# Kernel tuning notes

Hardware: AMD Instinct MI355X
Metric: run time of the kernel (lower is better)

## Reference

```python
import jax, jax.numpy as jnp
import numpy as np

N = 4096      # nodes (= maxlen)
E = 4096      # hyperedges
NFEAT = 512
NHID = 512
NHEAD = 8
DK = 64
DV = 64
NLAYER = 4
NCLASS = 16
GAMMA = 0.5
LN_EPS = 1e-5


def _incidence(key):
    # sparse-ish binary incidence matrix with no empty rows/cols
    H = (jax.random.uniform(key, (N, E)) < 0.004).astype(jnp.float32)
    H = H.at[jnp.arange(N), jnp.arange(N) % E].set(1.0)   # every node in >=1 edge
    H = H.at[jnp.arange(E) % N, jnp.arange(E)].set(1.0)   # every edge has >=1 node
    return H


def setup_inputs() -> dict:
    key = jax.random.key(0)
    ks = jax.random.split(key, 16)
    s = 0.02
    inp = {
        "X0": jax.random.normal(ks[0], (N, NFEAT), jnp.float32),
        "H": _incidence(ks[1]),
        "w_feat": jax.random.normal(ks[2], (NFEAT, NHID), jnp.float32) * s,
        "b_feat": jnp.zeros((NHID,), jnp.float32),
        "Wq": jax.random.normal(ks[3], (NLAYER, NHID, NHEAD * DK), jnp.float32) * s,
        "bq": jnp.zeros((NLAYER, NHEAD * DK), jnp.float32),
        "Wk": jax.random.normal(ks[4], (NLAYER, NHID, NHEAD * DK), jnp.float32) * s,
        "bk": jnp.zeros((NLAYER, NHEAD * DK), jnp.float32),
        "Wv": jax.random.normal(ks[5], (NLAYER, NHID, NHEAD * DV), jnp.float32) * s,
        "bv": jnp.zeros((NLAYER, NHEAD * DV), jnp.float32),
        "Wo": jax.random.normal(ks[6], (NLAYER, NHEAD * DV, NHID), jnp.float32) * s,
        "bo": jnp.zeros((NLAYER, NHID), jnp.float32),
        "ln_g": jnp.ones((NLAYER, NHID), jnp.float32),
        "ln_b": jnp.zeros((NLAYER, NHID), jnp.float32),
        "prelu_a": jnp.full((NLAYER,), 0.25, jnp.float32),
        "w_cls": jax.random.normal(ks[7], (NHID, NCLASS), jnp.float32) * s,
        "b_cls": jnp.zeros((NCLASS,), jnp.float32),
    }
    return inp


def _laplace(H):
    # G = DV^-1/2 H W DE^-1 H^T DV^-1/2 with W = I (diag matmuls as broadcasts)
    DV_ = jnp.sum(H, axis=1)                 # [N]
    DE_ = jnp.sum(H, axis=0)                 # [E]
    dv2 = DV_ ** -0.5
    dv2 = dv2.at[0].set(1.0)                 # DV2[0,0] = 1 quirk
    M = (H * (1.0 / DE_)[None, :]) @ H.T     # [N, N]
    return dv2[:, None] * M * dv2[None, :]


def _layer_norm(x, g, b):
    mu = jnp.mean(x, axis=-1, keepdims=True)
    var = jnp.mean((x - mu) ** 2, axis=-1, keepdims=True)
    return (x - mu) * jax.lax.rsqrt(var + LN_EPS) * g + b


def _encoder_layer(x, G, Wq, bq, Wk, bk, Wv, bv, Wo, bo, g, b, a):
    n = x.shape[0]
    q = (x @ Wq + bq).reshape(n, NHEAD, DK)
    k = (x @ Wk + bk).reshape(n, NHEAD, DK)
    v = (x @ Wv + bv).reshape(n, NHEAD, DV)
    scores = jnp.einsum("nhd,mhd->hnm", q, k) / np.sqrt(DK).astype(np.float32)
    attn = jax.nn.softmax(scores, axis=-1)                       # [h, n, n]
    blend = attn * GAMMA + G[None, :, :] * (1.0 - GAMMA)
    ctx = jnp.einsum("hnm,mhd->nhd", blend, v).reshape(n, NHEAD * DV)
    out = _layer_norm(ctx @ Wo + bo + x, g, b)                   # residual = V = x
    out = jnp.where(out >= 0, out, a * out)                      # PReLU (scalar a)
    return out  # dropout is identity at eval


def reference(X0, H, w_feat, b_feat, Wq, bq, Wk, bk, Wv, bv, Wo, bo,
              ln_g, ln_b, prelu_a, w_cls, b_cls):
    G = _laplace(H)
    x = X0 @ w_feat + b_feat
    for i in range(NLAYER):
        x = _encoder_layer(x, G, Wq[i], bq[i], Wk[i], bk[i], Wv[i], bv[i],
                           Wo[i], bo[i], ln_g[i], ln_b[i], prelu_a[i])
    logits = x @ w_cls + b_cls
    return jax.nn.log_softmax(logits, axis=1)
```

## Files before the change

### kernel.cpp

```cpp
#include <hip/hip_runtime.h>
#include <stdint.h>
#include <stddef.h>

typedef unsigned short u16;
typedef __attribute__((ext_vector_type(8))) short short8;
typedef __attribute__((ext_vector_type(4))) float floatx4;

#define NN 4096
#define FD 512
#define NLAYER 4
#define NCLASS 16

__device__ __forceinline__ float b2f(u16 u) {
  union { unsigned int i; float f; } x; x.i = ((unsigned int)u) << 16; return x.f;
}
__device__ __forceinline__ u16 f2b(float f) {
  union { float f; unsigned int i; } x; x.f = f;
  unsigned int r = x.i + 0x7fffu + ((x.i >> 16) & 1u);
  return (u16)(r >> 16);
}
__device__ __forceinline__ int is_f32(const void* Hraw) {
  return ((const u16*)Hraw)[0] == 0;
}
__device__ __forceinline__ float rload(const void* p, size_t i, int f) {
  if (f) { union { unsigned int i; float x; } u; u.i = ((const unsigned int*)p)[i]; return u.x; }
  return b2f(((const u16*)p)[i]);
}
__device__ __forceinline__ void gl2lds16(const void* g, void* l) {
  __builtin_amdgcn_global_load_lds((const __attribute__((address_space(1))) void*)g,
                                   (__attribute__((address_space(3))) void*)l, 16, 0, 0);
}

__global__ __launch_bounds__(256) void gemm_qkv(
    const u16* __restrict__ A, const u16* __restrict__ B, u16* __restrict__ qk,
    u16* __restrict__ vb, u16* __restrict__ vT, int K, long boff,
    const void* __restrict__ bq, const void* __restrict__ bk, const void* __restrict__ bv,
    const void* __restrict__ Hflag)
{
  __shared__ __align__(16) u16 As[64 * 32];
  __shared__ __align__(16) u16 Bs[128 * 32];
  __shared__ u16 Ts[4][16 * 17];
  const int tid = threadIdx.x;
  const int wave = tid >> 6, lane = tid & 63;
  const int wr = (wave >> 1) * 32, wc = (wave & 1) * 64;
  const int srow = lane >> 2;
  const int scol = (((lane & 3) ^ (srow & 3)) * 8);
  const int q4 = lane >> 4, l15 = lane & 15;
  const int sg = l15 & 3;

  floatx4 acc[2][4] = {};
  const u16* Ag = A + (size_t)(blockIdx.y * 64) * K;
  const u16* Bg = B + (size_t)(blockIdx.x * 128) * K;

  for (int k0 = 0; k0 < K; k0 += 32) {
    gl2lds16(Ag + (size_t)(wave * 16 + srow) * K + k0 + scol, &As[wave * 512]);
#pragma unroll
    for (int t = 0; t < 2; t++) {
      const int s = wave * 2 + t;
      gl2lds16(Bg + (size_t)(s * 16 + srow) * K + k0 + scol, &Bs[s * 512]);
    }
    __syncthreads();
    short8 af[2], bf[4];
#pragma unroll
    for (int mt = 0; mt < 2; mt++)
      af[mt] = *(const short8*)&As[(wr + mt * 16 + l15) * 32 + ((q4 ^ sg) * 8)];
#pragma unroll
    for (int nt = 0; nt < 4; nt++)
      bf[nt] = *(const short8*)&Bs[(wc + nt * 16 + l15) * 32 + ((q4 ^ sg) * 8)];
#pragma unroll
    for (int mt = 0; mt < 2; mt++)
#pragma unroll
      for (int nt = 0; nt < 4; nt++)
        acc[mt][nt] = __builtin_amdgcn_mfma_f32_16x16x32_bf16(af[mt], bf[nt], acc[mt][nt], 0, 0, 0);
    __syncthreads();
  }

  const int fl = is_f32(Hflag);
  const int buf = blockIdx.x >> 2;
  const void* bptr = (buf == 0) ? bq : (buf == 1) ? bk : bv;
  const int colbase = (blockIdx.x & 3) * 128;
  const int rowblk = blockIdx.y * 64;

  if (buf < 2) {
    u16* out = qk + (size_t)buf * 2097152;
#pragma unroll
    for (int mt = 0; mt < 2; mt++)
#pragma unroll
      for (int nt = 0; nt < 4; nt++)
#pragma unroll
        for (int r = 0; r < 4; r++) {
          const int row = rowblk + wr + mt * 16 + q4 * 4 + r;
          const int col = colbase + wc + nt * 16 + l15;
          out[(size_t)row * 512 + col] = f2b(acc[mt][nt][r] + rload(bptr, (size_t)boff + col, fl));
        }
  } else {
#pragma unroll
    for (int mt = 0; mt < 2; mt++)
#pragma unroll
      for (int nt = 0; nt < 4; nt++) {
#pragma unroll
        for (int r = 0; r < 4; r++) {
          const int row = rowblk + wr + mt * 16 + q4 * 4 + r;
          const int col = colbase + wc + nt * 16 + l15;
          const u16 val = f2b(acc[mt][nt][r] + rload(bptr, (size_t)boff + col, fl));
          vb[(size_t)row * 512 + col] = val;
          Ts[wave][(q4 * 4 + r) * 17 + l15] = val;
        }
#pragma unroll
        for (int r = 0; r < 4; r++) {
          const u16 tv = Ts[wave][l15 * 17 + q4 * 4 + r];
          const int vrow = colbase + wc + nt * 16 + q4 * 4 + r;
          const int vcol = rowblk + wr + mt * 16 + l15;
          vT[(size_t)vrow * NN + vcol] = tv;
        }
      }
  }
}

template<int EP>
__global__ __launch_bounds__(256) void gemm64_bt(
    const u16* __restrict__ A, const u16* __restrict__ B, u16* __restrict__ C,
    int M, int N, int K,
    const void* __restrict__ bias, long boff,
    const u16* __restrict__ add,
    const void* __restrict__ Hflag)
{
  __shared__ __align__(16) u16 As[64 * 32];
  __shared__ __align__(16) u16 Bs[128 * 32];
  const int tid = threadIdx.x;
  const int wave = tid >> 6, lane = tid & 63;
  const int wr = (wave >> 1) * 32, wc = (wave & 1) * 64;
  const int srow = lane >> 2;
  const int scol = (((lane & 3) ^ (srow & 3)) * 8);
  const int q4 = lane >> 4, l15 = lane & 15;
  const int sg = l15 & 3;

  floatx4 acc[2][4] = {};
  const u16* Ag = A + (size_t)(blockIdx.y * 64) * K;
  const u16* Bg = B + (size_t)(blockIdx.x * 128) * K;

  for (int k0 = 0; k0 < K; k0 += 32) {
    gl2lds16(Ag + (size_t)(wave * 16 + srow) * K + k0 + scol, &As[wave * 512]);
#pragma unroll
    for (int t = 0; t < 2; t++) {
      const int s = wave * 2 + t;
      gl2lds16(Bg + (size_t)(s * 16 + srow) * K + k0 + scol, &Bs[s * 512]);
    }
    __syncthreads();
    short8 af[2], bf[4];
#pragma unroll
    for (int mt = 0; mt < 2; mt++)
      af[mt] = *(const short8*)&As[(wr + mt * 16 + l15) * 32 + ((q4 ^ sg) * 8)];
#pragma unroll
    for (int nt = 0; nt < 4; nt++)
      bf[nt] = *(const short8*)&Bs[(wc + nt * 16 + l15) * 32 + ((q4 ^ sg) * 8)];
#pragma unroll
    for (int mt = 0; mt < 2; mt++)
#pragma unroll
      for (int nt = 0; nt < 4; nt++)
        acc[mt][nt] = __builtin_amdgcn_mfma_f32_16x16x32_bf16(af[mt], bf[nt], acc[mt][nt], 0, 0, 0);
    __syncthreads();
  }

  const int fl = is_f32(Hflag);
#pragma unroll
  for (int mt = 0; mt < 2; mt++)
#pragma unroll
    for (int nt = 0; nt < 4; nt++)
#pragma unroll
      for (int r = 0; r < 4; r++) {
        const int row = blockIdx.y * 64 + wr + mt * 16 + q4 * 4 + r;
        const int col = blockIdx.x * 128 + wc + nt * 16 + l15;
        float v = acc[mt][nt][r];
        if (EP == 2) v += rload(bias, (size_t)boff + col, fl);
        if (EP == 4) v += rload(bias, (size_t)boff + col, fl) + b2f(add[(size_t)row * N + col]);
        C[(size_t)row * N + col] = f2b(v);
      }
}

__global__ __launch_bounds__(256) void flash_attn(
    const u16* __restrict__ q, const u16* __restrict__ k,
    const u16* __restrict__ vT, u16* __restrict__ O0, u16* __restrict__ O1,
    float* __restrict__ lp)
{
  __shared__ __align__(16) u16 Qs[128 * 64];
  __shared__ __align__(16) u16 Ks[2][64 * 64], Vs[2][64 * 64];
  __shared__ __align__(16) u16 Ps[4][32 * 72];
  const int tid = threadIdx.x, wave = tid >> 6, lane = tid & 63;
  const int h = blockIdx.y, q0 = blockIdx.x * 128, z = blockIdx.z;
  const int jbase = z * 2048;
  const int r8 = lane >> 3;
  const int c8 = (((lane & 7) ^ r8) * 8);
  const int q4 = lane >> 4, l15 = lane & 15;
  const int sw = l15 & 7;

#pragma unroll
  for (int t = 0; t < 4; t++) {
    const int s = wave * 4 + t;
    gl2lds16(q + (size_t)(q0 + s * 8 + r8) * FD + h * 64 + c8, &Qs[s * 512]);
  }
#pragma unroll
  for (int t = 0; t < 2; t++) {
    const int s = wave * 2 + t;
    gl2lds16(k + (size_t)(jbase + s * 8 + r8) * FD + h * 64 + c8, &Ks[0][s * 512]);
    gl2lds16(vT + (size_t)(h * 64 + s * 8 + r8) * NN + jbase + c8, &Vs[0][s * 512]);
  }
  __syncthreads();
  short8 aq[2][2];
#pragma unroll
  for (int mt = 0; mt < 2; mt++) {
    aq[mt][0] = *(const short8*)&Qs[(wave * 32 + mt * 16 + l15) * 64 + ((q4 ^ sw) * 8)];
    aq[mt][1] = *(const short8*)&Qs[(wave * 32 + mt * 16 + l15) * 64 + (((q4 + 4) ^ sw) * 8)];
  }
  short8 vone;
#pragma unroll
  for (int j = 0; j < 8; j++) vone[j] = (short)0x3F80;

  floatx4 O[2][4] = {};
  floatx4 lacc[2] = {};

  for (int jt = 0; jt < 32; jt++) {
    const int cur = jt & 1;
    if (jt + 1 < 32) {
      const int nb = cur ^ 1;
      const int j0 = jbase + (jt + 1) * 64;
#pragma unroll
      for (int t = 0; t < 2; t++) {
        const int s = wave * 2 + t;
        gl2lds16(k + (size_t)(j0 + s * 8 + r8) * FD + h * 64 + c8, &Ks[nb][s * 512]);
        gl2lds16(vT + (size_t)(h * 64 + s * 8 + r8) * NN + j0 + c8, &Vs[nb][s * 512]);
      }
    }
    floatx4 sacc[2][4] = {};
#pragma unroll
    for (int nt = 0; nt < 4; nt++) {
      const short8 bk0 = *(const short8*)&Ks[cur][(nt * 16 + l15) * 64 + ((q4 ^ sw) * 8)];
      const short8 bk1 = *(const short8*)&Ks[cur][(nt * 16 + l15) * 64 + (((q4 + 4) ^ sw) * 8)];
#pragma unroll
      for (int mt = 0; mt < 2; mt++) {
        sacc[mt][nt] = __builtin_amdgcn_mfma_f32_16x16x32_bf16(aq[mt][0], bk0, sacc[mt][nt], 0, 0, 0);
        sacc[mt][nt] = __builtin_amdgcn_mfma_f32_16x16x32_bf16(aq[mt][1], bk1, sacc[mt][nt], 0, 0, 0);
      }
    }
#pragma unroll
    for (int mt = 0; mt < 2; mt++)
#pragma unroll
      for (int nt = 0; nt < 4; nt++)
#pragma unroll
        for (int r = 0; r < 4; r++) {
          const float pv = __expf(fmaf(sacc[mt][nt][r], 0.125f, -10.f));
          Ps[wave][(mt * 16 + q4 * 4 + r) * 72 + nt * 16 + l15] =
              (u16)(__float_as_uint(pv) >> 16);
        }
#pragma unroll
    for (int kk = 0; kk < 2; kk++) {
      short8 ap[2];
#pragma unroll
      for (int mt = 0; mt < 2; mt++)
        ap[mt] = *(const short8*)&Ps[wave][(mt * 16 + l15) * 72 + kk * 32 + q4 * 8];
#pragma unroll
      for (int dt = 0; dt < 4; dt++) {
        const short8 bv = *(const short8*)&Vs[cur][(dt * 16 + l15) * 64 + (((kk * 4 + q4) ^ sw) * 8)];
#pragma unroll
        for (int mt = 0; mt < 2; mt++)
          O[mt][dt] = __builtin_amdgcn_mfma_f32_16x16x32_bf16(ap[mt], bv, O[mt][dt], 0, 0, 0);
      }
#pragma unroll
      for (int mt = 0; mt < 2; mt++)
        lacc[mt] = __builtin_amdgcn_mfma_f32_16x16x32_bf16(ap[mt], vone, lacc[mt], 0, 0, 0);
    }
    __syncthreads();
  }
  u16* Op = z ? O1 : O0;
#pragma unroll
  for (int mt = 0; mt < 2; mt++) {
#pragma unroll
    for (int dt = 0; dt < 4; dt++)
#pragma unroll
      for (int r = 0; r < 4; r++)
        Op[(size_t)(q0 + wave * 32 + mt * 16 + q4 * 4 + r) * FD + h * 64 + dt * 16 + l15] =
            f2b(O[mt][dt][r]);
    if (l15 == 0)
#pragma unroll
      for (int r = 0; r < 4; r++)
        lp[z * 32768 + h * 4096 + q0 + wave * 32 + mt * 16 + q4 * 4 + r] = lacc[mt][r];
  }
}

__global__ __launch_bounds__(256) void spmm_edge(
    const int* __restrict__ offC, const int* __restrict__ nodeList,
    const float* __restrict__ invDE, const float* __restrict__ dv2,
    const u16* __restrict__ vb, float* __restrict__ b)
{
  const int wave = threadIdx.x >> 6, lane = threadIdx.x & 63;
  const int e = blockIdx.x * 4 + wave;
  const int beg = offC[e], end = offC[e + 1];
  float acc[8] = {};
  for (int j = beg; j < end; j++) {
    const int i = nodeList[j];
    const float dvi = dv2[i];
    const short8 row = *(const short8*)&vb[(size_t)i * 512 + lane * 8];
#pragma unroll
    for (int t = 0; t < 8; t++) acc[t] += dvi * b2f((u16)row[t]);
  }
  const float s = invDE[e];
  float4* out = (float4*)&b[(size_t)e * 512 + lane * 8];
  float4 o0, o1;
  o0.x = acc[0] * s; o0.y = acc[1] * s; o0.z = acc[2] * s; o0.w = acc[3] * s;
  o1.x = acc[4] * s; o1.y = acc[5] * s; o1.z = acc[6] * s; o1.w = acc[7] * s;
  out[0] = o0; out[1] = o1;
}

__global__ __launch_bounds__(256) void spmm_node(
    const int* __restrict__ offR, const int* __restrict__ edgeList,
    const float* __restrict__ dv2, const float* __restrict__ b,
    const u16* __restrict__ O0, const u16* __restrict__ O1,
    const float* __restrict__ lp, u16* __restrict__ ctx)
{
  const int wave = threadIdx.x >> 6, lane = threadIdx.x & 63;
  const int i = blockIdx.x * 4 + wave;
  const int beg = offR[i], end = offR[i + 1];
  float acc[8] = {};
  for (int j = beg; j < end; j++) {
    const int e = edgeList[j];
    const float4* bp = (const float4*)&b[(size_t)e * 512 + lane * 8];
    const float4 b0 = bp[0], b1 = bp[1];
    acc[0] += b0.x; acc[1] += b0.y; acc[2] += b0.z; acc[3] += b0.w;
    acc[4] += b1.x; acc[5] += b1.y; acc[6] += b1.z; acc[7] += b1.w;
  }
  const int h = lane >> 3;
  const float invl = 1.f / (lp[h * 4096 + i] + lp[32768 + h * 4096 + i]);
  const float dvi = dv2[i];
  const short8 a0 = *(const short8*)&O0[(size_t)i * 512 + lane * 8];
  const short8 a1 = *(const short8*)&O1[(size_t)i * 512 + lane * 8];
  short8 o;
#pragma unroll
  for (int t = 0; t < 8; t++)
    o[t] = (short)f2b(0.5f * (dvi * acc[t] + (b2f((u16)a0[t]) + b2f((u16)a1[t])) * invl));
  *(short8*)&ctx[(size_t)i * 512 + lane * 8] = o;
}

__global__ __launch_bounds__(256) void degrees_pass1(
    const void* __restrict__ H, float* __restrict__ colpart,
    float* __restrict__ rowsum) {
  __shared__ float cs[NN];
  __shared__ float wsum[16][4];
  const int f = is_f32(H);
  const int tid = threadIdx.x, wave = tid >> 6, lane = tid & 63;
  for (int i = tid; i < NN; i += 256) cs[i] = 0.f;
  __syncthreads();
  const int r0 = blockIdx.x * 16;
  for (int rr = 0; rr < 16; rr++) {
    const size_t rowbase = (size_t)(r0 + rr) * NN;
    float rs = 0.f;
#pragma unroll
    for (int j = 0; j < 16; j++) {
      const int c = tid + j * 256;
      const float v = rload(H, rowbase + c, f);
      cs[c] += v;
      rs += v;
    }
#pragma unroll
    for (int off = 1; off < 64; off <<= 1) rs += __shfl_xor(rs, off);
    if (lane == 0) wsum[rr][wave] = rs;
  }
  __syncthreads();
  if (tid < 16)
    rowsum[r0 + tid] = wsum[tid][0] + wsum[tid][1] + wsum[tid][2] + wsum[tid][3];
  float* cp = colpart + (size_t)blockIdx.x * NN;
  for (int i = tid; i < NN; i += 256) cp[i] = cs[i];
}

__global__ __launch_bounds__(256) void finalize_degrees(
    const float* __restrict__ colpart, float* __restrict__ invDE,
    const float* __restrict__ rowsum, float* __restrict__ dv2,
    float* __restrict__ colsum) {
  __shared__ float red[4][64];
  const int tid = threadIdx.x;
  const int c = tid & 63, pc = tid >> 6;
  const int col = blockIdx.x * 64 + c;
  float s = 0.f;
  for (int p = pc * 64; p < pc * 64 + 64; p++) s += colpart[(size_t)p * NN + col];
  red[pc][c] = s;
  const int r = blockIdx.x * 256 + tid;
  if (r < NN) dv2[r] = (r == 0) ? 1.f : rsqrtf(rowsum[r]);
  __syncthreads();
  if (pc == 0) {
    const float tot = red[0][c] + red[1][c] + red[2][c] + red[3][c];
    colsum[col] = tot;
    invDE[col] = 1.f / tot;
  }
}

__global__ __launch_bounds__(256) void build_offsets(
    const float* __restrict__ rowsum, const float* __restrict__ colsum,
    int* __restrict__ offR, int* __restrict__ offC,
    int* __restrict__ curR, int* __restrict__ curC)
{
  __shared__ int part[256];
  const int tid = threadIdx.x;
  for (int half = 0; half < 2; half++) {
    const float* src = half ? colsum : rowsum;
    int* off = half ? offC : offR;
    int* cur = half ? curC : curR;
    int local[16]; int s = 0;
#pragma unroll
    for (int j = 0; j < 16; j++) { local[j] = s; s += (int)(src[tid * 16 + j] + 0.5f); }
    part[tid] = s;
    __syncthreads();
    for (int d = 1; d < 256; d <<= 1) {
      const int v = (tid >= d) ? part[tid - d] : 0;
      __syncthreads();
      part[tid] += v;
      __syncthreads();
    }
    const int pre = (tid == 0) ? 0 : part[tid - 1];
#pragma unroll
    for (int j = 0; j < 16; j++) {
      const int o = pre + local[j];
      off[tid * 16 + j] = o;
      cur[tid * 16 + j] = o;
    }
    if (tid == 255) off[4096] = part[255];
    __syncthreads();
  }
}

__global__ void fill_csr(const void* __restrict__ H,
                         int* __restrict__ curR, int* __restrict__ curC,
                         int* __restrict__ edgeList, int* __restrict__ nodeList)
{
  const int f = is_f32(H);
  const size_t g = (size_t)blockIdx.x * 256 + threadIdx.x;
  const size_t stride = (size_t)gridDim.x * 256;
  for (size_t idx = g; idx < (size_t)NN * NN; idx += stride) {
    if (rload(H, idx, f) != 0.f) {
      const int i = (int)(idx >> 12);
      const int e = (int)(idx & (NN - 1));
      edgeList[atomicAdd(&curR[i], 1)] = e;
      nodeList[atomicAdd(&curC[e], 1)] = i;
    }
  }
}

__global__ __launch_bounds__(256) void transpose_cvt(
    const void* __restrict__ in, long eoff, u16* __restrict__ out, int R, int C,
    const void* __restrict__ Hflag) {
  __shared__ u16 tile[32][33];
  const int f = is_f32(Hflag);
  const int tx = threadIdx.x & 31, ty = threadIdx.x >> 5;
  const int bx = blockIdx.x, by = blockIdx.y;
#pragma unroll
  for (int kk = 0; kk < 4; kk++)
    tile[ty + kk * 8][tx] =
        f2b(rload(in, (size_t)eoff + (size_t)(by * 32 + ty + kk * 8) * C + bx * 32 + tx, f));
  __syncthreads();
#pragma unroll
  for (int kk = 0; kk < 4; kk++)
    out[(size_t)(bx * 32 + ty + kk * 8) * R + by * 32 + tx] = tile[tx][ty + kk * 8];
}

__global__ __launch_bounds__(256) void transpose_cvt4(
    const void* __restrict__ Wq, const void* __restrict__ Wk,
    const void* __restrict__ Wv, const void* __restrict__ Wo,
    long eoff, u16* __restrict__ wTs, const void* __restrict__ Hflag) {
  __shared__ u16 tile[32][33];
  const int z = blockIdx.z;
  const void* in = (z == 0) ? Wq : (z == 1) ? Wk : (z == 2) ? Wv : Wo;
  u16* out = wTs + (size_t)z * 262144;
  const int f = is_f32(Hflag);
  const int tx = threadIdx.x & 31, ty = threadIdx.x >> 5;
  const int bx = blockIdx.x, by = blockIdx.y;
#pragma unroll
  for (int kk = 0; kk < 4; kk++)
    tile[ty + kk * 8][tx] =
        f2b(rload(in, (size_t)eoff + (size_t)(by * 32 + ty + kk * 8) * 512 + bx * 32 + tx, f));
  __syncthreads();
#pragma unroll
  for (int kk = 0; kk < 4; kk++)
    out[(size_t)(bx * 32 + ty + kk * 8) * 512 + by * 32 + tx] = tile[tx][ty + kk * 8];
}

__global__ void convert_flat(const void* __restrict__ in, u16* __restrict__ out, int n,
                             const void* __restrict__ Hflag) {
  const int f = is_f32(Hflag);
  const int g = blockIdx.x * 256 + threadIdx.x;
  const int stride = gridDim.x * 256;
  for (int i = g; i < n; i += stride) out[i] = f2b(rload(in, i, f));
}

__global__ __launch_bounds__(256) void ln_prelu(
    const u16* __restrict__ pre, const void* __restrict__ g, const void* __restrict__ bb,
    const void* __restrict__ aa, int lidx, u16* __restrict__ X,
    const void* __restrict__ Hflag) {
  const int f = is_f32(Hflag);
  const int tid = threadIdx.x, wave = tid >> 6, lane = tid & 63;
  const int row = blockIdx.x * 4 + wave;
  const short8 raw = *(const short8*)(pre + (size_t)row * FD + lane * 8);
  float v[8], s = 0.f;
#pragma unroll
  for (int j = 0; j < 8; j++) { v[j] = b2f((u16)raw[j]); s += v[j]; }
#pragma unroll
  for (int off = 1; off < 64; off <<= 1) s += __shfl_xor(s, off);
  const float mu = s * (1.f / 512.f);
  float vs = 0.f;
#pragma unroll
  for (int j = 0; j < 8; j++) { const float d = v[j] - mu; vs += d * d; }
#pragma unroll
  for (int off = 1; off < 64; off <<= 1) vs += __shfl_xor(vs, off);
  const float rstd = rsqrtf(vs * (1.f / 512.f) + 1e-5f);
  const float a = rload(aa, lidx, f);
  short8 o;
#pragma unroll
  for (int j = 0; j < 8; j++) {
    float y = (v[j] - mu) * rstd * rload(g, (size_t)lidx * 512 + lane * 8 + j, f)
              + rload(bb, (size_t)lidx * 512 + lane * 8 + j, f);
    y = (y >= 0.f) ? y : a * y;
    o[j] = (short)f2b(y);
  }
  *(short8*)(X + (size_t)row * FD + lane * 8) = o;
}

__global__ __launch_bounds__(256) void cls_logsoftmax(
    const u16* __restrict__ X, const void* __restrict__ w, const void* __restrict__ bc,
    void* __restrict__ out, const void* __restrict__ Hflag) {
  __shared__ float wsm[FD * NCLASS];
  const int f = is_f32(Hflag);
  const int tid = threadIdx.x;
  for (int i = tid; i < FD * NCLASS; i += 256) wsm[i] = rload(w, i, f);
  __syncthreads();
  const int c = tid & 15;
  const int row = blockIdx.x * 16 + (tid >> 4);
  const u16* x = X + (size_t)row * FD;
  float z = rload(bc, c, f);
  for (int kk = 0; kk < FD; kk++) z += b2f(x[kk]) * wsm[kk * NCLASS + c];
  float mx = z;
#pragma unroll
  for (int off = 1; off < 16; off <<= 1) mx = fmaxf(mx, __shfl_xor(mx, off));
  float se = __expf(z - mx);
#pragma unroll
  for (int off = 1; off < 16; off <<= 1) se += __shfl_xor(se, off);
  const float val = z - mx - logf(se);
  if (f) ((float*)out)[(size_t)row * NCLASS + c] = val;
  else   ((u16*)out)[(size_t)row * NCLASS + c] = f2b(val);
}

extern "C" void kernel_launch(void* const* d_in, const int* in_sizes, int n_in,
                              void* d_out, int out_size, void* d_ws, size_t ws_size,
                              hipStream_t stream) {
  const void* X0     = d_in[0];
  const void* H      = d_in[1];
  const void* w_feat = d_in[2];
  const void* b_feat = d_in[3];
  const void* Wq     = d_in[4];
  const void* bq     = d_in[5];
  const void* Wk     = d_in[6];
  const void* bk     = d_in[7];
  const void* Wv     = d_in[8];
  const void* bv     = d_in[9];
  const void* Wo     = d_in[10];
  const void* bo     = d_in[11];
  const void* ln_g   = d_in[12];
  const void* ln_b   = d_in[13];
  const void* pa     = d_in[14];
  const void* w_cls  = d_in[15];
  const void* b_cls  = d_in[16];

  char* ws = (char*)d_ws;
  char* r1 = ws;
  int* offR      = (int*)(r1 + (0 << 10));
  int* offC      = (int*)(r1 + (32 << 10));
  int* curR      = (int*)(r1 + (64 << 10));
  int* curC      = (int*)(r1 + (96 << 10));
  int* edgeList  = (int*)(r1 + ((size_t)1 << 20));
  int* nodeList  = (int*)(r1 + ((size_t)4 << 20));
  float* bbuf    = (float*)(r1 + ((size_t)8 << 20));
  u16* vb        = (u16*)(r1 + ((size_t)16 << 20));
  float* colpart = (float*)(r1 + ((size_t)20 << 20));

  char* r2  = ws + ((size_t)32 << 20);
  u16* qb     = (u16*)(r2 + ((size_t)0  << 20));
  u16* Opart0 = (u16*)(r2 + ((size_t)8  << 20));
  u16* vTb    = (u16*)(r2 + ((size_t)12 << 20));
  u16* ctx    = (u16*)(r2 + ((size_t)16 << 20));
  u16* X      = (u16*)(r2 + ((size_t)20 << 20));
  u16* wTs    = (u16*)(r2 + ((size_t)24 << 20));
  u16* Opart1 = (u16*)(r2 + ((size_t)26 << 20));
  float* lpart = (float*)(r2 + ((size_t)30 << 20));
  u16* opre = qb;
  u16* X0b  = Opart0;

  float* dv2    = (float*)d_out;
  float* invDE  = dv2 + 4096;
  float* rowsum = dv2 + 8192;
  float* colsum = dv2 + 12288;

  degrees_pass1<<<256, 256, 0, stream>>>(H, colpart, rowsum);
  finalize_degrees<<<64, 256, 0, stream>>>(colpart, invDE, rowsum, dv2, colsum);
  build_offsets<<<1, 256, 0, stream>>>(rowsum, colsum, offR, offC, curR, curC);
  fill_csr<<<2048, 256, 0, stream>>>(H, curR, curC, edgeList, nodeList);

  convert_flat<<<2048, 256, 0, stream>>>(X0, X0b, NN * FD, H);
  transpose_cvt<<<dim3(16, 16), 256, 0, stream>>>(w_feat, 0, wTs, 512, 512, H);
  gemm64_bt<2><<<dim3(4, 64), 256, 0, stream>>>(X0b, wTs, X, NN, FD, FD, b_feat, 0, nullptr, H);

  for (int l = 0; l < NLAYER; l++) {
    const long lw = (long)l * 262144;
    transpose_cvt4<<<dim3(16, 16, 4), 256, 0, stream>>>(Wq, Wk, Wv, Wo, lw, wTs, H);

    gemm_qkv<<<dim3(12, 64), 256, 0, stream>>>(X, wTs, qb, vb, vTb, FD, (long)l * 512, bq, bk, bv, H);
    flash_attn<<<dim3(32, 8, 2), 256, 0, stream>>>(qb, qb + 2097152, vTb, Opart0, Opart1, lpart);
    spmm_edge<<<1024, 256, 0, stream>>>(offC, nodeList, invDE, dv2, vb, bbuf);
    spmm_node<<<1024, 256, 0, stream>>>(offR, edgeList, dv2, bbuf, Opart0, Opart1, lpart, ctx);
    gemm64_bt<4><<<dim3(4, 64), 256, 0, stream>>>(ctx, wTs + 3 * 262144, opre, NN, FD, FD, bo, (long)l * 512, X, H);
    ln_prelu<<<1024, 256, 0, stream>>>(opre, ln_g, ln_b, pa, l, X, H);
  }

  cls_logsoftmax<<<256, 256, 0, stream>>>(X, w_cls, b_cls, d_out, H);
}
```

Baseline: 883.1 us.

## Split flash attention key range three ways and alias Q and P shared memory

Flash attention now splits the 4096 keys into three chunks (22, 21 and 21 tiles) instead of two, launching 768 blocks rather than 512 for better CU fill on the 256-CU device. Shared memory is reduced by letting the per-wave P scratch reuse the Q staging buffer once Q is loaded into registers, guarded by an extra barrier, which may allow more resident blocks. spmm_node now combines three partial outputs and three row sums, adding one more bf16 partial read. The third partial buffer shares workspace with colpart, which relies on colpart being dead after the degree setup.

```diff
diff --git a/kernel.cpp b/kernel.cpp
--- a/kernel.cpp
+++ b/kernel.cpp
@@ -181,23 +181,25 @@
 __global__ __launch_bounds__(256) void flash_attn(
     const u16* __restrict__ q, const u16* __restrict__ k,
     const u16* __restrict__ vT, u16* __restrict__ O0, u16* __restrict__ O1,
-    float* __restrict__ lp)
+    u16* __restrict__ O2, float* __restrict__ lp)
 {
-  __shared__ __align__(16) u16 Qs[128 * 64];
+  __shared__ __align__(16) u16 QP[9216];
   __shared__ __align__(16) u16 Ks[2][64 * 64], Vs[2][64 * 64];
-  __shared__ __align__(16) u16 Ps[4][32 * 72];
   const int tid = threadIdx.x, wave = tid >> 6, lane = tid & 63;
   const int h = blockIdx.y, q0 = blockIdx.x * 128, z = blockIdx.z;
-  const int jbase = z * 2048;
+  const int jstart = (z == 0) ? 0 : (22 + 21 * (z - 1));
+  const int ntiles = (z == 0) ? 22 : 21;
+  const int jbase = jstart * 64;
   const int r8 = lane >> 3;
   const int c8 = (((lane & 7) ^ r8) * 8);
   const int q4 = lane >> 4, l15 = lane & 15;
   const int sw = l15 & 7;
+  u16* Ps = QP + wave * 2304;
 
 #pragma unroll
   for (int t = 0; t < 4; t++) {
     const int s = wave * 4 + t;
-    gl2lds16(q + (size_t)(q0 + s * 8 + r8) * FD + h * 64 + c8, &Qs[s * 512]);
+    gl2lds16(q + (size_t)(q0 + s * 8 + r8) * FD + h * 64 + c8, &QP[s * 512]);
   }
 #pragma unroll
   for (int t = 0; t < 2; t++) {
@@ -209,9 +211,10 @@
   short8 aq[2][2];
 #pragma unroll
   for (int mt = 0; mt < 2; mt++) {
-    aq[mt][0] = *(const short8*)&Qs[(wave * 32 + mt * 16 + l15) * 64 + ((q4 ^ sw) * 8)];
-    aq[mt][1] = *(const short8*)&Qs[(wave * 32 + mt * 16 + l15) * 64 + (((q4 + 4) ^ sw) * 8)];
-  }
+    aq[mt][0] = *(const short8*)&QP[(wave * 32 + mt * 16 + l15) * 64 + ((q4 ^ sw) * 8)];
+    aq[mt][1] = *(const short8*)&QP[(wave * 32 + mt * 16 + l15) * 64 + (((q4 + 4) ^ sw) * 8)];
+  }
+  __syncthreads();
   short8 vone;
 #pragma unroll
   for (int j = 0; j < 8; j++) vone[j] = (short)0x3F80;
@@ -219,9 +222,9 @@
   floatx4 O[2][4] = {};
   floatx4 lacc[2] = {};
 
-  for (int jt = 0; jt < 32; jt++) {
+  for (int jt = 0; jt < ntiles; jt++) {
     const int cur = jt & 1;
-    if (jt + 1 < 32) {
+    if (jt + 1 < ntiles) {
       const int nb = cur ^ 1;
       const int j0 = jbase + (jt + 1) * 64;
 #pragma unroll
@@ -249,7 +252,7 @@
 #pragma unroll
         for (int r = 0; r < 4; r++) {
           const float pv = __expf(fmaf(sacc[mt][nt][r], 0.125f, -10.f));
-          Ps[wave][(mt * 16 + q4 * 4 + r) * 72 + nt * 16 + l15] =
+          Ps[(mt * 16 + q4 * 4 + r) * 72 + nt * 16 + l15] =
               (u16)(__float_as_uint(pv) >> 16);
         }
 #pragma unroll
@@ -257,7 +260,7 @@
       short8 ap[2];
 #pragma unroll
       for (int mt = 0; mt < 2; mt++)
-        ap[mt] = *(const short8*)&Ps[wave][(mt * 16 + l15) * 72 + kk * 32 + q4 * 8];
+        ap[mt] = *(const short8*)&Ps[(mt * 16 + l15) * 72 + kk * 32 + q4 * 8];
 #pragma unroll
       for (int dt = 0; dt < 4; dt++) {
         const short8 bv = *(const short8*)&Vs[cur][(dt * 16 + l15) * 64 + (((kk * 4 + q4) ^ sw) * 8)];
@@ -271,7 +274,7 @@
     }
     __syncthreads();
   }
-  u16* Op = z ? O1 : O0;
+  u16* Op = (z == 0) ? O0 : (z == 1) ? O1 : O2;
 #pragma unroll
   for (int mt = 0; mt < 2; mt++) {
 #pragma unroll
@@ -314,7 +317,7 @@
 __global__ __launch_bounds__(256) void spmm_node(
     const int* __restrict__ offR, const int* __restrict__ edgeList,
     const float* __restrict__ dv2, const float* __restrict__ b,
-    const u16* __restrict__ O0, const u16* __restrict__ O1,
+    const u16* __restrict__ O0, const u16* __restrict__ O1, const u16* __restrict__ O2,
     const float* __restrict__ lp, u16* __restrict__ ctx)
 {
   const int wave = threadIdx.x >> 6, lane = threadIdx.x & 63;
@@ -329,14 +332,17 @@
     acc[4] += b1.x; acc[5] += b1.y; acc[6] += b1.z; acc[7] += b1.w;
   }
   const int h = lane >> 3;
-  const float invl = 1.f / (lp[h * 4096 + i] + lp[32768 + h * 4096 + i]);
+  const float invl = 1.f / (lp[h * 4096 + i] + lp[32768 + h * 4096 + i] +
+                            lp[65536 + h * 4096 + i]);
   const float dvi = dv2[i];
   const short8 a0 = *(const short8*)&O0[(size_t)i * 512 + lane * 8];
   const short8 a1 = *(const short8*)&O1[(size_t)i * 512 + lane * 8];
+  const short8 a2 = *(const short8*)&O2[(size_t)i * 512 + lane * 8];
   short8 o;
 #pragma unroll
   for (int t = 0; t < 8; t++)
-    o[t] = (short)f2b(0.5f * (dvi * acc[t] + (b2f((u16)a0[t]) + b2f((u16)a1[t])) * invl));
+    o[t] = (short)f2b(0.5f * (dvi * acc[t] +
+        (b2f((u16)a0[t]) + b2f((u16)a1[t]) + b2f((u16)a2[t])) * invl));
   *(short8*)&ctx[(size_t)i * 512 + lane * 8] = o;
 }
 
@@ -577,6 +583,7 @@
   float* bbuf    = (float*)(r1 + ((size_t)8 << 20));
   u16* vb        = (u16*)(r1 + ((size_t)16 << 20));
   float* colpart = (float*)(r1 + ((size_t)20 << 20));
+  u16* Opart2    = (u16*)(r1 + ((size_t)20 << 20));
 
   char* r2  = ws + ((size_t)32 << 20);
   u16* qb     = (u16*)(r2 + ((size_t)0  << 20));
@@ -609,9 +616,9 @@
     transpose_cvt4<<<dim3(16, 16, 4), 256, 0, stream>>>(Wq, Wk, Wv, Wo, lw, wTs, H);
 
     gemm_qkv<<<dim3(12, 64), 256, 0, stream>>>(X, wTs, qb, vb, vTb, FD, (long)l * 512, bq, bk, bv, H);
-    flash_attn<<<dim3(32, 8, 2), 256, 0, stream>>>(qb, qb + 2097152, vTb, Opart0, Opart1, lpart);
+    flash_attn<<<dim3(32, 8, 3), 256, 0, stream>>>(qb, qb + 2097152, vTb, Opart0, Opart1, Opart2, lpart);
     spmm_edge<<<1024, 256, 0, stream>>>(offC, nodeList, invDE, dv2, vb, bbuf);
-    spmm_node<<<1024, 256, 0, stream>>>(offR, edgeList, dv2, bbuf, Opart0, Opart1, lpart, ctx);
+    spmm_node<<<1024, 256, 0, stream>>>(offR, edgeList, dv2, bbuf, Opart0, Opart1, Opart2, lpart, ctx);
     gemm64_bt<4><<<dim3(4, 64), 256, 0, stream>>>(ctx, wTs + 3 * 262144, opre, NN, FD, FD, bo, (long)l * 512, X, H);
     ln_prelu<<<1024, 256, 0, stream>>>(opre, ln_g, ln_b, pa, l, X, H);
   }
```

After: 843.0 us. -4.5%, faster.
